# Performance work log

Hardware: AMD Instinct MI355X
Metric: run time of the kernel (lower is better)

## Reference

```python
import jax, jax.numpy as jnp
import numpy as np

L, D, H, KVH, DH, F, V, SMAX, T = 4, 2048, 16, 8, 128, 6144, 32000, 2048, 1024
EPS = 1e-6
ROPE_THETA = 1e6


def rotate_half(x, axis=-1):
    x1, x2 = jnp.split(x, 2, axis=axis)
    return jnp.concatenate((-x2, x1), axis=axis)


def rms(x, w):
    return w * (x / jnp.sqrt(jnp.mean(x * x, axis=-1, keepdims=True) + EPS))


def setup_inputs() -> dict:
    key = jax.random.key(0)
    ks = jax.random.split(key, 16)
    s = 0.02
    inv_freq = 1.0 / (ROPE_THETA ** (jnp.arange(0, DH, 2, dtype=jnp.float32) / DH))
    ang = jnp.arange(SMAX, dtype=jnp.float32)[:, None] * inv_freq[None, :]  # [SMAX, DH/2]
    cos_emb = jnp.concatenate([jnp.cos(ang), jnp.cos(ang)], axis=-1)  # [SMAX, DH]
    sin_emb = jnp.concatenate([jnp.sin(ang), jnp.sin(ang)], axis=-1)
    sf = DH ** (-0.25)  # scale_factor pre-baked into q_norm/k_norm weights
    return {
        "key_buffer": jnp.zeros((L, KVH, 1, DH, SMAX), jnp.float32),
        "value_buffer": jnp.zeros((L, KVH, 1, SMAX, DH), jnp.float32),
        "input_ids": jax.random.randint(ks[0], (1, T), 0, V, dtype=jnp.int32),
        "attention_mask": jnp.ones((1, T, T), jnp.float32),
        "past_len": 0,
        "embed_data": jax.random.randint(ks[1], (V, D), 0, 256).astype(jnp.uint8),
        "embed_scale": jax.random.uniform(ks[2], (V, 1), jnp.float32, 0.001, 0.02),
        "embed_zero": jax.random.normal(ks[3], (V, 1), jnp.float32) * 0.1,
        "cos_emb": cos_emb,
        "sin_emb": sin_emb,
        "w_in_ln": jnp.ones((L, D), jnp.float32),
        "Wq": jax.random.normal(ks[4], (L, D, H * DH), jnp.float32) * s,
        "Wk": jax.random.normal(ks[5], (L, D, KVH * DH), jnp.float32) * s,
        "Wv": jax.random.normal(ks[6], (L, D, KVH * DH), jnp.float32) * s,
        "w_q_norm": jnp.full((L, DH), sf, jnp.float32),
        "w_k_norm": jnp.full((L, DH), sf, jnp.float32),
        "Wo": jax.random.normal(ks[7], (L, H * DH, D), jnp.float32) * s,
        "w_post_ln": jnp.ones((L, D), jnp.float32),
        "Wgate": jax.random.normal(ks[8], (L, D, F), jnp.float32) * s,
        "Wup": jax.random.normal(ks[9], (L, D, F), jnp.float32) * s,
        "Wdown": jax.random.normal(ks[10], (L, F, D), jnp.float32) * s,
        "w_final_norm": jnp.ones((D,), jnp.float32),
        "W_lm": jax.random.normal(ks[11], (D, V), jnp.float32) * s,
    }


def reference(key_buffer, value_buffer, input_ids, attention_mask, past_len,
              embed_data, embed_scale, embed_zero, cos_emb, sin_emb,
              w_in_ln, Wq, Wk, Wv, w_q_norm, w_k_norm, Wo, w_post_ln,
              Wgate, Wup, Wdown, w_final_norm, W_lm):
    new_len = input_ids.shape[1]
    end = past_len + new_len  # static (past_len is a Python int)
    cos_q = cos_emb[past_len:end]  # [T, DH]
    sin_q = sin_emb[past_len:end]
    # uint8 embedding dequant: e * scale + zero_point
    hidden = embed_data[input_ids].astype(jnp.float32) * embed_scale[input_ids] + embed_zero[input_ids]  # [1,T,D]
    # causal mask: (1 - tril) * -128, sliced to [1, new_len, end], times user mask
    rows = jnp.arange(new_len) + past_len
    cols = jnp.arange(end)
    mask = jnp.where(cols[None, :] <= rows[:, None], 0.0, -128.0)[None] * attention_mask  # [1,T,end]
    G = H // KVH
    for i in range(L):
        hn = rms(hidden, w_in_ln[i])[0]  # [T, D]
        q = (hn @ Wq[i]).reshape(new_len, H, DH)
        q = jnp.transpose(rms(q, w_q_norm[i]), (1, 0, 2))  # [H,T,DH] (sqrt(scale) baked in w_q_norm)
        k = (hn @ Wk[i]).reshape(new_len, KVH, DH)
        k = jnp.transpose(rms(k, w_k_norm[i]), (1, 2, 0))  # [KVH,DH,T]
        v = jnp.transpose((hn @ Wv[i]).reshape(new_len, KVH, DH), (1, 0, 2))  # [KVH,T,DH]
        # RoPE on keys (rotate along DH axis=1)
        k = k * cos_q.T + rotate_half(k, axis=1) * sin_q.T
        key_buffer = jax.lax.dynamic_update_slice(key_buffer, k[None, :, None], (i, 0, 0, 0, past_len))
        value_buffer = jax.lax.dynamic_update_slice(value_buffer, v[None, :, None], (i, 0, 0, past_len, 0))
        # GQA expand: each kv head repeated G times consecutively
        k_exp = jnp.repeat(key_buffer[i, :, 0, :, :end], G, axis=0)  # [H,DH,end]
        v_exp = jnp.repeat(value_buffer[i, :, 0, :end, :], G, axis=0)  # [H,end,DH]
        q_rot = q * cos_q[None] + rotate_half(q, axis=-1) * sin_q[None]
        scores = jnp.einsum('htd,hds->hts', q_rot, k_exp) + mask
        attn = jax.nn.softmax(scores, axis=-1)
        ctx = jnp.transpose(jnp.einsum('hts,hsd->htd', attn, v_exp), (1, 0, 2)).reshape(1, new_len, H * DH)
        hidden = hidden + ctx @ Wo[i]
        hn2 = rms(hidden, w_post_ln[i])
        hidden = hidden + (jax.nn.silu(hn2 @ Wgate[i]) * (hn2 @ Wup[i])) @ Wdown[i]
    last = rms(hidden[:, -1], w_final_norm)  # [1, D]
    logits = last @ W_lm  # [1, V]
    tok_id = jnp.argmax(logits, axis=-1, keepdims=True).astype(jnp.int32)
    new_seq_len = jnp.array([end], dtype=jnp.int32)
    return (tok_id, key_buffer, value_buffer, new_seq_len)
```

## Files before the change

kernel.cpp:

```cpp
#include <hip/hip_runtime.h>
#include <cstdint>

#define L_ 4
#define D_ 2048
#define H_ 16
#define KVH_ 8
#define DH_ 128
#define F_ 6144
#define V_ 32000
#define SMAX_ 2048
#define T_ 1024
#define EPS_ 1e-6f
#define QB 64
#define SB 128

typedef unsigned short u16;
typedef unsigned int u32;
typedef float fvec4 __attribute__((ext_vector_type(4)));
typedef float f32x4 __attribute__((ext_vector_type(4)));
typedef __bf16 bf16x8 __attribute__((ext_vector_type(8)));

__device__ __forceinline__ u16 f2bf(float f) {
  union { float f; u32 u; } a; a.f = f;
  u32 u = a.u;
  return (u16)((u + 0x7FFFu + ((u >> 16) & 1u)) >> 16);
}

__device__ __forceinline__ void gld16(const void* g, void* l) {
  __builtin_amdgcn_global_load_lds(
      (const __attribute__((address_space(1))) void*)g,
      (__attribute__((address_space(3))) void*)l, 16, 0, 0);
}

__device__ __forceinline__ float blk_sum(float v, volatile float* sm) {
#pragma unroll
  for (int m = 32; m; m >>= 1) v += __shfl_xor(v, m);
  if ((threadIdx.x & 63) == 0) sm[threadIdx.x >> 6] = v;
  __syncthreads();
  v = sm[0] + sm[1] + sm[2] + sm[3];
  __syncthreads();
  return v;
}

__global__ void embed_k(const int* __restrict__ ids, const void* __restrict__ edata,
                        const float* __restrict__ esc, const float* __restrict__ ez,
                        float* __restrict__ hidden)
{
  const int* ei = (const int*)edata;
  int chk = ei[threadIdx.x & 63];
  bool ok = ((unsigned)chk) <= 255u;
  bool is_i32 = (__ballot(ok) == ~0ULL);
  int t = blockIdx.x;
  int id = ids[t];
  float sc = esc[id], zp = ez[id];
  size_t base = (size_t)id * D_;
  const uint8_t* eb = (const uint8_t*)edata;
  for (int d = threadIdx.x; d < D_; d += 256) {
    float e = is_i32 ? (float)ei[base + d] : (float)eb[base + d];
    hidden[(size_t)t * D_ + d] = e * sc + zp;
  }
}

__global__ __launch_bounds__(256)
void convT2_k(const float* __restrict__ W0, const float* __restrict__ W1,
              const float* __restrict__ W2,
              int x1, int x2, int N0, int N1, int N2,
              int r0, int r1, int r2, int K, u16* __restrict__ WT, int gu)
{
  __shared__ float tile[64][65];
  int x = blockIdx.x, k0 = blockIdx.y * 64;
  const float* W; int N, nb, rb;
  if (x < x1)      { W = W0; N = N0; nb = x;      rb = r0; }
  else if (x < x2) { W = W1; N = N1; nb = x - x1; rb = r1; }
  else             { W = W2; N = N2; nb = x - x2; rb = r2; }
  int n0 = nb * 64;
  int tid = threadIdx.x;
  int lk = tid >> 4, n4 = (tid & 15) * 4;
#pragma unroll
  for (int i = 0; i < 4; ++i) {
    int kr = i * 16 + lk;
    fvec4 v = *(const fvec4*)(W + (size_t)(k0 + kr) * N + n0 + n4);
#pragma unroll
    for (int j = 0; j < 4; ++j) tile[n4 + j][kr] = v[j];
  }
  __syncthreads();
  int n = tid >> 2, kq = (tid & 3) * 16;
  int f = n0 + n;
  int row = gu ? (rb + ((f >> 4) << 5) + (f & 15)) : (rb + f);
  union { u16 h[16]; uint4 q[2]; } o;
#pragma unroll
  for (int i = 0; i < 16; ++i) o.h[i] = f2bf(tile[n][kq + i]);
  u16* op = WT + (size_t)row * K + k0 + kq;
  *(uint4*)op = o.q[0];
  *(uint4*)(op + 8) = o.q[1];
}

template<int COMB>
__global__ void rms_k(float* __restrict__ x, const float* __restrict__ p0,
                      const float* __restrict__ p1, const float* __restrict__ w,
                      u16* __restrict__ out)
{
  __shared__ float sm[4];
  int t = blockIdx.x;
  fvec4* xr = (fvec4*)(x + (size_t)t * D_);
  fvec4 v0 = xr[threadIdx.x], v1 = xr[threadIdx.x + 256];
  if (COMB) {
    const fvec4* a = (const fvec4*)(p0 + (size_t)t * D_);
    const fvec4* b = (const fvec4*)(p1 + (size_t)t * D_);
    v0 += a[threadIdx.x] + b[threadIdx.x];
    v1 += a[threadIdx.x + 256] + b[threadIdx.x + 256];
    xr[threadIdx.x] = v0;
    xr[threadIdx.x + 256] = v1;
  }
  float s = v0[0]*v0[0] + v0[1]*v0[1] + v0[2]*v0[2] + v0[3]*v0[3]
          + v1[0]*v1[0] + v1[1]*v1[1] + v1[2]*v1[2] + v1[3]*v1[3];
  s = blk_sum(s, sm);
  float inv = rsqrtf(s * (1.f / D_) + EPS_);
  const fvec4* wr = (const fvec4*)w;
  fvec4 w0 = wr[threadIdx.x], w1 = wr[threadIdx.x + 256];
  u16* orow = out + (size_t)t * D_;
  uint2 o0, o1;
  o0.x = (u32)f2bf(w0[0]*v0[0]*inv) | ((u32)f2bf(w0[1]*v0[1]*inv) << 16);
  o0.y = (u32)f2bf(w0[2]*v0[2]*inv) | ((u32)f2bf(w0[3]*v0[3]*inv) << 16);
  o1.x = (u32)f2bf(w1[0]*v1[0]*inv) | ((u32)f2bf(w1[1]*v1[1]*inv) << 16);
  o1.y = (u32)f2bf(w1[2]*v1[2]*inv) | ((u32)f2bf(w1[3]*v1[3]*inv) << 16);
  *(uint2*)(orow + threadIdx.x * 4) = o0;
  *(uint2*)(orow + (threadIdx.x + 256) * 4) = o1;
}

template<int EPI>
__global__ __launch_bounds__(256)
void gemm_bt(const u16* __restrict__ A, const u16* __restrict__ B,
             float* __restrict__ Cf, u16* __restrict__ Cb,
             int K, int Ks, int ldC, long long zStride)
{
  __shared__ u16 lA[128 * 64];
  __shared__ u16 lB[128 * 64];
  const u16* Ab = A + (size_t)blockIdx.y * 128 * K;
  const u16* Bb = B + (size_t)blockIdx.x * 128 * K;
  int kz = blockIdx.z * Ks;

  int tid = threadIdx.x;
  int l = tid & 63;
  int wid = tid >> 6;
  int wr = wid >> 1, wc = wid & 1;
  int lrow = l & 15, lk = l >> 4;

  f32x4 acc[4][4] = {};

  for (int k0 = 0; k0 < Ks; k0 += 64) {
#pragma unroll
    for (int r = 0; r < 4; ++r) {
      int c = r * 256 + tid;
      int row = c >> 3, g = c & 7;
      int kel = kz + k0 + ((g ^ (row & 7)) << 3);
      gld16(Ab + (size_t)row * K + kel, (char*)lA + c * 16);
      gld16(Bb + (size_t)row * K + kel, (char*)lB + c * 16);
    }
    __syncthreads();
#pragma unroll
    for (int kk = 0; kk < 2; ++kk) {
      bf16x8 av[4], bv[4];
      int kbyte = (kk * 32 + lk * 8) * 2;
#pragma unroll
      for (int m = 0; m < 4; ++m) {
        int row = wr * 64 + m * 16 + lrow;
        int byt = (row * 128 + kbyte) ^ ((row & 7) << 4);
        av[m] = *(const bf16x8*)((const char*)lA + byt);
      }
#pragma unroll
      for (int n = 0; n < 4; ++n) {
        int row = wc * 64 + n * 16 + lrow;
        int byt = (row * 128 + kbyte) ^ ((row & 7) << 4);
        bv[n] = *(const bf16x8*)((const char*)lB + byt);
      }
#pragma unroll
      for (int m = 0; m < 4; ++m)
#pragma unroll
        for (int n = 0; n < 4; ++n)
          acc[m][n] = __builtin_amdgcn_mfma_f32_16x16x32_bf16(av[m], bv[n], acc[m][n], 0, 0, 0);
    }
    __syncthreads();
  }

  int grow0 = blockIdx.y * 128 + wr * 64 + lk * 4;
  if (EPI == 3) {
    int fcol0 = blockIdx.x * 64 + wc * 32 + lrow;
#pragma unroll
    for (int m = 0; m < 4; ++m)
#pragma unroll
      for (int np = 0; np < 2; ++np)
#pragma unroll
        for (int r = 0; r < 4; ++r) {
          float g = acc[m][2 * np][r], u = acc[m][2 * np + 1][r];
          float val = g / (1.f + __expf(-g)) * u;
          Cb[(size_t)(grow0 + m * 16 + r) * ldC + fcol0 + np * 16] = f2bf(val);
        }
    return;
  }
  float* Cz = Cf + (long long)blockIdx.z * zStride;
  int gcol0 = blockIdx.x * 128 + wc * 64 + lrow;
#pragma unroll
  for (int m = 0; m < 4; ++m)
#pragma unroll
    for (int n = 0; n < 4; ++n)
#pragma unroll
      for (int r = 0; r < 4; ++r) {
        size_t off = (size_t)(grow0 + m * 16 + r) * ldC + gcol0 + n * 16;
        Cz[off] = acc[m][n][r];
      }
}

__global__ __launch_bounds__(256)
void qkvpost_k(const float* __restrict__ p0, const float* __restrict__ p1,
               const float* __restrict__ wq, const float* __restrict__ wk,
               const float* __restrict__ cosT, const float* __restrict__ sinT,
               const int* __restrict__ plp,
               u16* __restrict__ qr, u16* __restrict__ kr, u16* __restrict__ vT,
               float* __restrict__ key_out, float* __restrict__ val_out)
{
  __shared__ float tile[64][132];
  int t0 = blockIdx.x * 64;
  int z = blockIdx.y;
  int pl = plp[0];
  int tid = threadIdx.x;
  int cb = z < 16 ? z * 128 : (z < 24 ? 2048 + (z - 16) * 128 : 3072 + (z - 24) * 128);

  {
    int r = tid >> 5;
    int c = (tid & 31) * 4;
#pragma unroll
    for (int i = 0; i < 8; ++i) {
      int row = i * 8 + r;
      size_t off = (size_t)(t0 + row) * 4096 + cb + c;
      fvec4 v = *(const fvec4*)(p0 + off) + *(const fvec4*)(p1 + off);
      *(fvec4*)&tile[row][c] = v;
    }
  }
  __syncthreads();

  if (z < 24) {
    int row = tid >> 2, q = tid & 3;
    int dbase = q * 32, pbase = (q ^ 2) * 32;
    const float* wn = z < 16 ? wq : wk;
    float sgn = (q < 2) ? -1.f : 1.f;
    fvec4 xv[8];
    float ss = 0.f;
#pragma unroll
    for (int j = 0; j < 8; ++j) {
      xv[j] = *(const fvec4*)&tile[row][dbase + j * 4];
      ss += xv[j][0]*xv[j][0] + xv[j][1]*xv[j][1] + xv[j][2]*xv[j][2] + xv[j][3]*xv[j][3];
    }
    ss += __shfl_xor(ss, 1);
    ss += __shfl_xor(ss, 2);
    float inv = rsqrtf(ss * (1.f / 128.f) + EPS_);
    int p = pl + t0 + row;
    float rv[32];
#pragma unroll
    for (int j = 0; j < 8; ++j) {
      fvec4 xo = *(const fvec4*)&tile[row][pbase + j * 4];
      fvec4 wv = *(const fvec4*)(wn + dbase + j * 4);
      fvec4 wo = *(const fvec4*)(wn + pbase + j * 4);
      fvec4 cs = *(const fvec4*)(cosT + (size_t)p * 128 + dbase + j * 4);
      fvec4 sn = *(const fvec4*)(sinT + (size_t)p * 128 + dbase + j * 4);
#pragma unroll
      for (int e = 0; e < 4; ++e) {
        float xn = wv[e] * xv[j][e] * inv;
        float xp = wo[e] * xo[e] * inv;
        rv[j * 4 + e] = xn * cs[e] + sgn * xp * sn[e];
      }
    }
    union { u32 w[8]; uint4 q4[2]; } ob;
    u16* orow = (z < 16 ? qr + ((size_t)z * T_ + t0 + row) * 128
                        : kr + ((size_t)(z - 16) * T_ + t0 + row) * 128) + dbase;
#pragma unroll
    for (int j = 0; j < 8; ++j)
      ob.w[j] = (u32)f2bf(rv[2 * j]) | ((u32)f2bf(rv[2 * j + 1]) << 16);
    *(uint4*)orow = ob.q4[0];
#pragma unroll
    for (int j = 0; j < 8; ++j)
      ob.w[j] = (u32)f2bf(rv[16 + 2 * j]) | ((u32)f2bf(rv[17 + 2 * j]) << 16);
    *(uint4*)(orow + 16) = ob.q4[0];

    if (z >= 16) {
      __syncthreads();
#pragma unroll
      for (int j = 0; j < 8; ++j) {
        fvec4 v; v[0] = rv[j*4]; v[1] = rv[j*4+1]; v[2] = rv[j*4+2]; v[3] = rv[j*4+3];
        *(fvec4*)&tile[row][dbase + j * 4] = v;
      }
      __syncthreads();
      int d = tid >> 1, cc = (tid & 1) * 32;
      float* kp = key_out + ((size_t)(z - 16) * 128 + d) * SMAX_ + pl + t0 + cc;
      if ((pl & 3) == 0) {
#pragma unroll
        for (int j4 = 0; j4 < 8; ++j4) {
          fvec4 v;
#pragma unroll
          for (int e = 0; e < 4; ++e) v[e] = tile[cc + j4 * 4 + e][d];
          *(fvec4*)(kp + j4 * 4) = v;
        }
      } else {
        for (int j = 0; j < 32; ++j) kp[j] = tile[cc + j][d];
      }
    }
  } else {
    int kv = z - 24;
    int row = tid >> 2, q = tid & 3;
    float* vp = val_out + ((size_t)kv * SMAX_ + pl + t0 + row) * 128 + q * 32;
#pragma unroll
    for (int j = 0; j < 8; ++j)
      *(fvec4*)(vp + j * 4) = *(const fvec4*)&tile[row][q * 32 + j * 4];
    int d = tid >> 1, cc = (tid & 1) * 32;
    union { u32 w[8]; uint4 q4[2]; } ob;
    u16* tp = vT + ((size_t)kv * 128 + d) * T_ + t0 + cc;
#pragma unroll
    for (int j = 0; j < 8; ++j)
      ob.w[j] = (u32)f2bf(tile[cc + 2 * j][d]) | ((u32)f2bf(tile[cc + 2 * j + 1][d]) << 16);
    *(uint4*)tp = ob.q4[0];
    *(uint4*)(tp + 8) = ob.q4[1];
  }
}

__global__ __launch_bounds__(256)
void flash_k(const u16* __restrict__ qr, const u16* __restrict__ kr,
             const u16* __restrict__ vTb, const float* __restrict__ am,
             const int* __restrict__ plp, u16* __restrict__ ctx)
{
  __shared__ u16 lQ[QB * DH_];
  __shared__ u16 lKV[SB * DH_];
  __shared__ u16 lP[QB * SB];
  __shared__ float lScale[QB];
  __shared__ float lSum[QB];

  int qt = gridDim.x - 1 - blockIdx.x;
  int h = blockIdx.y;
  int kvh = h >> 1;
  int pl = plp[0];
  int tid = threadIdx.x;
  int l = tid & 63, w = tid >> 6;
  int lrow = l & 15, lk = l >> 4;

  const u16* Qb = qr + ((size_t)h * T_ + qt * QB) * DH_;
  const u16* Kb = kr + (size_t)kvh * T_ * DH_;
  const u16* Vb = vTb + (size_t)kvh * DH_ * T_;

#pragma unroll
  for (int r = 0; r < 4; ++r) {
    int c = r * 256 + tid;
    int row = c >> 4, g = c & 15;
    gld16(Qb + (size_t)row * DH_ + ((g ^ (row & 7)) << 3), (char*)lQ + c * 16);
  }

  float m_run = -3.0e38f, l_run = 0.f;
  f32x4 acc_o[4][2] = {};

  int t_lo = qt * QB;
  int s_hi = min(T_, t_lo + QB + pl);
  int nt = (s_hi + SB - 1) / SB;
  int tcol = w * 16 + lrow;
  int tg = t_lo + tcol;

  for (int it = 0; it < nt; ++it) {
    int s0 = it * SB;
#pragma unroll
    for (int r = 0; r < 8; ++r) {
      int c = r * 256 + tid;
      int row = c >> 4, g = c & 15;
      gld16(Kb + (size_t)(s0 + row) * DH_ + ((g ^ (row & 7)) << 3), (char*)lKV + c * 16);
    }
    __syncthreads();

    f32x4 acc_s[8] = {};
#pragma unroll
    for (int kk = 0; kk < 4; ++kk) {
      int kbyte = kk * 64 + lk * 16;
      int trow = w * 16 + lrow;
      bf16x8 bq = *(const bf16x8*)((const char*)lQ + ((trow * 256 + kbyte) ^ ((trow & 7) << 4)));
#pragma unroll
      for (int m = 0; m < 8; ++m) {
        int srow = m * 16 + lrow;
        bf16x8 ak = *(const bf16x8*)((const char*)lKV + ((srow * 256 + kbyte) ^ ((srow & 7) << 4)));
        acc_s[m] = __builtin_amdgcn_mfma_f32_16x16x32_bf16(ak, bq, acc_s[m], 0, 0, 0);
      }
    }
    __syncthreads();

#pragma unroll
    for (int r = 0; r < 8; ++r) {
      int c = r * 256 + tid;
      int row = c >> 4, g = c & 15;
      gld16(Vb + (size_t)row * T_ + s0 + ((g ^ (row & 7)) << 3), (char*)lKV + c * 16);
    }

    bool full = (s0 + SB <= t_lo + pl + 1);
    float vmax = -3.0e38f;
    float sv[8][4];
    if (full) {
#pragma unroll
      for (int m = 0; m < 8; ++m)
#pragma unroll
        for (int r = 0; r < 4; ++r) {
          float val = acc_s[m][r]; sv[m][r] = val; vmax = fmaxf(vmax, val);
        }
    } else {
#pragma unroll
      for (int m = 0; m < 8; ++m) {
        int sg = s0 + m * 16 + lk * 4;
        fvec4 a4 = *(const fvec4*)(am + (size_t)tg * T_ + sg);
#pragma unroll
        for (int r = 0; r < 4; ++r) {
          float val = acc_s[m][r] + ((sg + r <= tg + pl) ? 0.f : -128.f * a4[r]);
          sv[m][r] = val; vmax = fmaxf(vmax, val);
        }
      }
    }
    vmax = fmaxf(vmax, __shfl_xor(vmax, 16));
    vmax = fmaxf(vmax, __shfl_xor(vmax, 32));
    float m_new = fmaxf(m_run, vmax);
    float corr = __expf(m_run - m_new);
    float psum = 0.f;
    u32 pw[8][2];
#pragma unroll
    for (int m = 0; m < 8; ++m) {
      float pq0 = __expf(sv[m][0] - m_new);
      float pq1 = __expf(sv[m][1] - m_new);
      float pq2 = __expf(sv[m][2] - m_new);
      float pq3 = __expf(sv[m][3] - m_new);
      psum += (pq0 + pq1) + (pq2 + pq3);
      pw[m][0] = (u32)f2bf(pq0) | ((u32)f2bf(pq1) << 16);
      pw[m][1] = (u32)f2bf(pq2) | ((u32)f2bf(pq3) << 16);
    }
    psum += __shfl_xor(psum, 16);
    psum += __shfl_xor(psum, 32);
    l_run = l_run * corr + psum;
    m_run = m_new;
    if (lk == 0) lScale[tcol] = corr;
#pragma unroll
    for (int m = 0; m < 8; ++m) {
      int byt = (tcol * 256 + m * 32 + lk * 8) ^ ((tcol & 7) << 4);
      *(uint2*)((char*)lP + byt) = make_uint2(pw[m][0], pw[m][1]);
    }
    __syncthreads();

#pragma unroll
    for (int m = 0; m < 4; ++m) {
      fvec4 c4 = *(const fvec4*)&lScale[m * 16 + lk * 4];
#pragma unroll
      for (int n = 0; n < 2; ++n)
#pragma unroll
        for (int r = 0; r < 4; ++r) acc_o[m][n][r] *= c4[r];
    }
#pragma unroll
    for (int kk = 0; kk < 4; ++kk) {
      int kbyte = kk * 64 + lk * 16;
      bf16x8 ap[4], bv[2];
#pragma unroll
      for (int m = 0; m < 4; ++m) {
        int trow = m * 16 + lrow;
        ap[m] = *(const bf16x8*)((const char*)lP + ((trow * 256 + kbyte) ^ ((trow & 7) << 4)));
      }
#pragma unroll
      for (int n = 0; n < 2; ++n) {
        int drow = w * 32 + n * 16 + lrow;
        bv[n] = *(const bf16x8*)((const char*)lKV + ((drow * 256 + kbyte) ^ ((drow & 7) << 4)));
      }
#pragma unroll
      for (int m = 0; m < 4; ++m)
#pragma unroll
        for (int n = 0; n < 2; ++n)
          acc_o[m][n] = __builtin_amdgcn_mfma_f32_16x16x32_bf16(ap[m], bv[n], acc_o[m][n], 0, 0, 0);
    }
    __syncthreads();
  }

  if (lk == 0) lSum[tcol] = l_run;
  __syncthreads();
#pragma unroll
  for (int m = 0; m < 4; ++m) {
    fvec4 s4 = *(const fvec4*)&lSum[m * 16 + lk * 4];
#pragma unroll
    for (int r = 0; r < 4; ++r) {
      float inv = 1.f / s4[r];
      int trow = t_lo + m * 16 + lk * 4 + r;
      u16* crow = ctx + (size_t)trow * (H_ * DH_) + h * DH_;
#pragma unroll
      for (int n = 0; n < 2; ++n) {
        int d = w * 32 + n * 16 + lrow;
        crow[d] = f2bf(acc_o[m][n][r] * inv);
      }
    }
  }
}

__global__ void frms_k(const float* __restrict__ x, const float* __restrict__ p0,
                       const float* __restrict__ p1, const float* __restrict__ w,
                       float* __restrict__ out)
{
  __shared__ float sm[4];
  float s = 0.f;
  for (int d = threadIdx.x; d < D_; d += 256) {
    float v = x[d] + p0[d] + p1[d];
    s += v * v;
  }
  s = blk_sum(s, sm);
  float inv = rsqrtf(s * (1.f / D_) + EPS_);
  for (int d = threadIdx.x; d < D_; d += 256)
    out[d] = w[d] * (x[d] + p0[d] + p1[d]) * inv;
}

__global__ void lmgemv_k(const float* __restrict__ last, const float* __restrict__ Wlm,
                         float* __restrict__ part)
{
  __shared__ float ls[256];
  int v = blockIdx.x * 256 + threadIdx.x;
  int c = blockIdx.y;
  ls[threadIdx.x] = last[c * 256 + threadIdx.x];
  __syncthreads();
  const float* Wp = Wlm + (size_t)c * 256 * V_ + v;
  float acc = 0.f;
#pragma unroll 8
  for (int d = 0; d < 256; d++) acc += ls[d] * Wp[(size_t)d * V_];
  part[(size_t)c * V_ + v] = acc;
}

__global__ void amax_part_k(const float* __restrict__ part, float2* __restrict__ out)
{
  __shared__ float sv[4];
  __shared__ int si[4];
  int v = blockIdx.x * 256 + threadIdx.x;
  float val = 0.f;
#pragma unroll
  for (int c = 0; c < 8; c++) val += part[(size_t)c * V_ + v];
  float bv = val; int bi = v;
#pragma unroll
  for (int m = 32; m; m >>= 1) {
    float ov = __shfl_xor(bv, m);
    int oi = __shfl_xor(bi, m);
    if (ov > bv || (ov == bv && oi < bi)) { bv = ov; bi = oi; }
  }
  if ((threadIdx.x & 63) == 0) { sv[threadIdx.x >> 6] = bv; si[threadIdx.x >> 6] = bi; }
  __syncthreads();
  if (threadIdx.x == 0) {
    for (int w = 1; w < 4; w++)
      if (sv[w] > bv || (sv[w] == bv && si[w] < bi)) { bv = sv[w]; bi = si[w]; }
    out[blockIdx.x] = make_float2(bv, (float)bi);
  }
}

__global__ void finalize_k(const float2* __restrict__ part, int np,
                           const int* __restrict__ plp, float* __restrict__ dout,
                           unsigned long long lastoff)
{
  if (threadIdx.x == 0) {
    float bv = part[0].x; int bi = (int)part[0].y;
    for (int b = 1; b < np; b++) {
      float v = part[b].x; int i = (int)part[b].y;
      if (v > bv || (v == bv && i < bi)) { bv = v; bi = i; }
    }
    dout[0] = (float)bi;
    dout[lastoff] = (float)(plp[0] + T_);
  }
}

extern "C" void kernel_launch(void* const* d_in, const int* in_sizes, int n_in,
                              void* d_out, int out_size, void* d_ws, size_t ws_size,
                              hipStream_t stream)
{
  (void)in_sizes; (void)n_in; (void)out_size; (void)ws_size;

  const float* key_in  = (const float*)d_in[0];
  const float* val_in  = (const float*)d_in[1];
  const int*   ids     = (const int*)d_in[2];
  const float* am      = (const float*)d_in[3];
  const int*   plp     = (const int*)d_in[4];
  const void*  edata   = d_in[5];
  const float* esc     = (const float*)d_in[6];
  const float* ez      = (const float*)d_in[7];
  const float* cosT    = (const float*)d_in[8];
  const float* sinT    = (const float*)d_in[9];
  const float* w_in_ln = (const float*)d_in[10];
  const float* Wq      = (const float*)d_in[11];
  const float* Wk      = (const float*)d_in[12];
  const float* Wv      = (const float*)d_in[13];
  const float* wqn     = (const float*)d_in[14];
  const float* wkn     = (const float*)d_in[15];
  const float* Wo      = (const float*)d_in[16];
  const float* wpost   = (const float*)d_in[17];
  const float* Wg      = (const float*)d_in[18];
  const float* Wu      = (const float*)d_in[19];
  const float* Wd      = (const float*)d_in[20];
  const float* wfin    = (const float*)d_in[21];
  const float* Wlm     = (const float*)d_in[22];

  float* out = (float*)d_out;
  const size_t KVN = (size_t)L_ * KVH_ * DH_ * SMAX_;
  float* key_out = out + 1;
  float* val_out = out + 1 + KVN;
  unsigned long long lastoff = 1 + 2 * KVN;

  char* ws = (char*)d_ws;
  u16*   wT     = (u16*)  (ws + 0);
  u16*   hn     = (u16*)  (ws + 50331648);
  float* P0     = (float*)(ws + 54525952);
  float* P1     = (float*)(ws + 71303168);
  u16*   qr     = (u16*)  (ws + 88080384);
  u16*   kr     = (u16*)  (ws + 92274688);
  u16*   vT     = (u16*)  (ws + 94371840);
  u16*   ctx    = (u16*)  (ws + 96468992);
  float* hidden = (float*)(ws + 100663296);
  u16*   mlp    = (u16*)  (ws + 109051904);
  float* last   = (float*)(ws + 121634816);
  float* lpart  = (float*)(ws + 121643008);
  float2* amaxp = (float2*)(ws + 122667008);

  const long long ZS = 4194304;

  hipMemcpyAsync(key_out, key_in, KVN * sizeof(float), hipMemcpyDeviceToDevice, stream);
  hipMemcpyAsync(val_out, val_in, KVN * sizeof(float), hipMemcpyDeviceToDevice, stream);
  embed_k<<<T_, 256, 0, stream>>>(ids, edata, esc, ez, hidden);

  for (int i = 0; i < L_; i++) {
    if (i == 0)
      rms_k<0><<<T_, 256, 0, stream>>>(hidden, nullptr, nullptr, w_in_ln, hn);
    else
      rms_k<1><<<T_, 256, 0, stream>>>(hidden, P0, P1, w_in_ln + (size_t)i * D_, hn);

    convT2_k<<<dim3(64, 32), 256, 0, stream>>>(
        Wq + (size_t)i * 4194304, Wk + (size_t)i * 2097152, Wv + (size_t)i * 2097152,
        32, 48, 2048, 1024, 1024, 0, 2048, 3072, 2048, wT, 0);
    gemm_bt<0><<<dim3(32, 8, 2), 256, 0, stream>>>(hn, wT, P0, nullptr, 2048, 1024, 4096, ZS);

    qkvpost_k<<<dim3(T_ / 64, 32), 256, 0, stream>>>(P0, P1,
        wqn + (size_t)i * DH_, wkn + (size_t)i * DH_, cosT, sinT, plp,
        qr, kr, vT,
        key_out + (size_t)i * KVH_ * DH_ * SMAX_,
        val_out + (size_t)i * KVH_ * SMAX_ * DH_);

    flash_k<<<dim3(T_ / QB, H_), 256, 0, stream>>>(qr, kr, vT, am, plp, ctx);

    convT2_k<<<dim3(32, 32), 256, 0, stream>>>(
        Wo + (size_t)i * 4194304, nullptr, nullptr,
        32, 64, 2048, 2048, 2048, 0, 0, 0, 2048, wT, 0);
    gemm_bt<0><<<dim3(16, 8, 2), 256, 0, stream>>>(ctx, wT, P0, nullptr, 2048, 1024, 2048, ZS);

    rms_k<1><<<T_, 256, 0, stream>>>(hidden, P0, P1, wpost + (size_t)i * D_, hn);

    convT2_k<<<dim3(192, 32), 256, 0, stream>>>(
        Wg + (size_t)i * 12582912, Wu + (size_t)i * 12582912, Wu + (size_t)i * 12582912,
        96, 192, 6144, 6144, 6144, 0, 16, 16, 2048, wT, 1);
    gemm_bt<3><<<dim3(96, 8, 1), 256, 0, stream>>>(hn, wT, nullptr, mlp, 2048, 2048, 6144, 0);

    convT2_k<<<dim3(32, 96), 256, 0, stream>>>(
        Wd + (size_t)i * 12582912, nullptr, nullptr,
        32, 64, 2048, 2048, 2048, 0, 0, 0, 6144, wT, 0);
    gemm_bt<0><<<dim3(16, 8, 2), 256, 0, stream>>>(mlp, wT, P0, nullptr, 6144, 3072, 2048, ZS);
  }

  frms_k<<<1, 256, 0, stream>>>(hidden + (size_t)(T_ - 1) * D_,
                                P0 + (size_t)(T_ - 1) * D_, P1 + (size_t)(T_ - 1) * D_,
                                wfin, last);
  lmgemv_k<<<dim3(V_ / 256, 8), 256, 0, stream>>>(last, Wlm, lpart);
  amax_part_k<<<V_ / 256, 256, 0, stream>>>(lpart, amaxp);
  finalize_k<<<1, 64, 0, stream>>>(amaxp, V_ / 256, plp, out, lastoff);
}
```

Baseline: 1.291 ms.

## Halve flash query tile, split S across waves, widen split-K to four partials

The flash attention kernel drops to 32-row query tiles, with the four waves split into two query groups by two key halves. Row max and sum are combined through shared memory, which doubles the number of blocks for better CU occupancy. The Wo and Wdown GEMMs now use four split-K partials instead of two, and the RMS kernels sum all four partials, raising parallelism at the cost of more partial-buffer traffic. The qkvpost kernel also adds the second 16-byte store for each output chunk, fixing previously unwritten elements.

```diff
diff --git a/kernel.cpp b/kernel.cpp
--- a/kernel.cpp
+++ b/kernel.cpp
@@ -11,8 +11,9 @@
 #define SMAX_ 2048
 #define T_ 1024
 #define EPS_ 1e-6f
-#define QB 64
+#define QB 32
 #define SB 128
+#define ZSE 4194304
 
 typedef unsigned short u16;
 typedef unsigned int u32;
@@ -95,20 +96,21 @@
   *(uint4*)(op + 8) = o.q[1];
 }
 
-template<int COMB>
-__global__ void rms_k(float* __restrict__ x, const float* __restrict__ p0,
-                      const float* __restrict__ p1, const float* __restrict__ w,
-                      u16* __restrict__ out)
+template<int NZ>
+__global__ void rms_k(float* __restrict__ x, const float* __restrict__ p,
+                      const float* __restrict__ w, u16* __restrict__ out)
 {
   __shared__ float sm[4];
   int t = blockIdx.x;
   fvec4* xr = (fvec4*)(x + (size_t)t * D_);
   fvec4 v0 = xr[threadIdx.x], v1 = xr[threadIdx.x + 256];
-  if (COMB) {
-    const fvec4* a = (const fvec4*)(p0 + (size_t)t * D_);
-    const fvec4* b = (const fvec4*)(p1 + (size_t)t * D_);
-    v0 += a[threadIdx.x] + b[threadIdx.x];
-    v1 += a[threadIdx.x + 256] + b[threadIdx.x + 256];
+  if (NZ > 0) {
+#pragma unroll
+    for (int z = 0; z < NZ; ++z) {
+      const fvec4* a = (const fvec4*)(p + (size_t)z * ZSE + (size_t)t * D_);
+      v0 += a[threadIdx.x];
+      v1 += a[threadIdx.x + 256];
+    }
     xr[threadIdx.x] = v0;
     xr[threadIdx.x + 256] = v1;
   }
@@ -277,10 +279,12 @@
     for (int j = 0; j < 8; ++j)
       ob.w[j] = (u32)f2bf(rv[2 * j]) | ((u32)f2bf(rv[2 * j + 1]) << 16);
     *(uint4*)orow = ob.q4[0];
+    *(uint4*)(orow + 8) = ob.q4[1];
 #pragma unroll
     for (int j = 0; j < 8; ++j)
       ob.w[j] = (u32)f2bf(rv[16 + 2 * j]) | ((u32)f2bf(rv[17 + 2 * j]) << 16);
     *(uint4*)(orow + 16) = ob.q4[0];
+    *(uint4*)(orow + 24) = ob.q4[1];
 
     if (z >= 16) {
       __syncthreads();
@@ -330,8 +334,10 @@
   __shared__ u16 lQ[QB * DH_];
   __shared__ u16 lKV[SB * DH_];
   __shared__ u16 lP[QB * SB];
+  __shared__ float lMax[2][2][16];
+  __shared__ float lSum[2][2][16];
   __shared__ float lScale[QB];
-  __shared__ float lSum[QB];
+  __shared__ float lFin[QB];
 
   int qt = gridDim.x - 1 - blockIdx.x;
   int h = blockIdx.y;
@@ -340,25 +346,26 @@
   int tid = threadIdx.x;
   int l = tid & 63, w = tid >> 6;
   int lrow = l & 15, lk = l >> 4;
+  int tb = w & 1, sh = w >> 1;
+  int tcol = tb * 16 + lrow;
 
   const u16* Qb = qr + ((size_t)h * T_ + qt * QB) * DH_;
   const u16* Kb = kr + (size_t)kvh * T_ * DH_;
   const u16* Vb = vTb + (size_t)kvh * DH_ * T_;
 
 #pragma unroll
-  for (int r = 0; r < 4; ++r) {
+  for (int r = 0; r < 2; ++r) {
     int c = r * 256 + tid;
     int row = c >> 4, g = c & 15;
     gld16(Qb + (size_t)row * DH_ + ((g ^ (row & 7)) << 3), (char*)lQ + c * 16);
   }
 
   float m_run = -3.0e38f, l_run = 0.f;
-  f32x4 acc_o[4][2] = {};
+  f32x4 acc_o[2][2] = {};
 
   int t_lo = qt * QB;
   int s_hi = min(T_, t_lo + QB + pl);
   int nt = (s_hi + SB - 1) / SB;
-  int tcol = w * 16 + lrow;
   int tg = t_lo + tcol;
 
   for (int it = 0; it < nt; ++it) {
@@ -371,15 +378,15 @@
     }
     __syncthreads();
 
-    f32x4 acc_s[8] = {};
+    f32x4 acc_s[4] = {};
 #pragma unroll
     for (int kk = 0; kk < 4; ++kk) {
       int kbyte = kk * 64 + lk * 16;
-      int trow = w * 16 + lrow;
+      int trow = tb * 16 + lrow;
       bf16x8 bq = *(const bf16x8*)((const char*)lQ + ((trow * 256 + kbyte) ^ ((trow & 7) << 4)));
 #pragma unroll
-      for (int m = 0; m < 8; ++m) {
-        int srow = m * 16 + lrow;
+      for (int m = 0; m < 4; ++m) {
+        int srow = sh * 64 + m * 16 + lrow;
         bf16x8 ak = *(const bf16x8*)((const char*)lKV + ((srow * 256 + kbyte) ^ ((srow & 7) << 4)));
         acc_s[m] = __builtin_amdgcn_mfma_f32_16x16x32_bf16(ak, bq, acc_s[m], 0, 0, 0);
       }
@@ -394,19 +401,19 @@
     }
 
     bool full = (s0 + SB <= t_lo + pl + 1);
+    float sv[4][4];
     float vmax = -3.0e38f;
-    float sv[8][4];
     if (full) {
 #pragma unroll
-      for (int m = 0; m < 8; ++m)
+      for (int m = 0; m < 4; ++m)
 #pragma unroll
         for (int r = 0; r < 4; ++r) {
           float val = acc_s[m][r]; sv[m][r] = val; vmax = fmaxf(vmax, val);
         }
     } else {
 #pragma unroll
-      for (int m = 0; m < 8; ++m) {
-        int sg = s0 + m * 16 + lk * 4;
+      for (int m = 0; m < 4; ++m) {
+        int sg = s0 + sh * 64 + m * 16 + lk * 4;
         fvec4 a4 = *(const fvec4*)(am + (size_t)tg * T_ + sg);
 #pragma unroll
         for (int r = 0; r < 4; ++r) {
@@ -417,34 +424,39 @@
     }
     vmax = fmaxf(vmax, __shfl_xor(vmax, 16));
     vmax = fmaxf(vmax, __shfl_xor(vmax, 32));
-    float m_new = fmaxf(m_run, vmax);
+    if (lk == 0) lMax[tb][sh][lrow] = vmax;
+    __syncthreads();
+
+    float om = fmaxf(lMax[tb][0][lrow], lMax[tb][1][lrow]);
+    float m_new = fmaxf(m_run, om);
     float corr = __expf(m_run - m_new);
     float psum = 0.f;
-    u32 pw[8][2];
-#pragma unroll
-    for (int m = 0; m < 8; ++m) {
-      float pq0 = __expf(sv[m][0] - m_new);
-      float pq1 = __expf(sv[m][1] - m_new);
-      float pq2 = __expf(sv[m][2] - m_new);
-      float pq3 = __expf(sv[m][3] - m_new);
-      psum += (pq0 + pq1) + (pq2 + pq3);
-      pw[m][0] = (u32)f2bf(pq0) | ((u32)f2bf(pq1) << 16);
-      pw[m][1] = (u32)f2bf(pq2) | ((u32)f2bf(pq3) << 16);
+    u32 pw[4][2];
+#pragma unroll
+    for (int m = 0; m < 4; ++m) {
+      float p0 = __expf(sv[m][0] - m_new);
+      float p1 = __expf(sv[m][1] - m_new);
+      float p2 = __expf(sv[m][2] - m_new);
+      float p3 = __expf(sv[m][3] - m_new);
+      psum += (p0 + p1) + (p2 + p3);
+      pw[m][0] = (u32)f2bf(p0) | ((u32)f2bf(p1) << 16);
+      pw[m][1] = (u32)f2bf(p2) | ((u32)f2bf(p3) << 16);
     }
     psum += __shfl_xor(psum, 16);
     psum += __shfl_xor(psum, 32);
-    l_run = l_run * corr + psum;
+    if (lk == 0) lSum[tb][sh][lrow] = psum;
+    if (lk == 0 && sh == 0) lScale[tcol] = corr;
+#pragma unroll
+    for (int m = 0; m < 4; ++m) {
+      int byt = (tcol * 256 + sh * 128 + m * 32 + lk * 8) ^ ((tcol & 7) << 4);
+      *(uint2*)((char*)lP + byt) = make_uint2(pw[m][0], pw[m][1]);
+    }
+    __syncthreads();
+
+    l_run = l_run * corr + lSum[tb][0][lrow] + lSum[tb][1][lrow];
     m_run = m_new;
-    if (lk == 0) lScale[tcol] = corr;
-#pragma unroll
-    for (int m = 0; m < 8; ++m) {
-      int byt = (tcol * 256 + m * 32 + lk * 8) ^ ((tcol & 7) << 4);
-      *(uint2*)((char*)lP + byt) = make_uint2(pw[m][0], pw[m][1]);
-    }
-    __syncthreads();
-
-#pragma unroll
-    for (int m = 0; m < 4; ++m) {
+#pragma unroll
+    for (int m = 0; m < 2; ++m) {
       fvec4 c4 = *(const fvec4*)&lScale[m * 16 + lk * 4];
 #pragma unroll
       for (int n = 0; n < 2; ++n)
@@ -454,9 +466,9 @@
 #pragma unroll
     for (int kk = 0; kk < 4; ++kk) {
       int kbyte = kk * 64 + lk * 16;
-      bf16x8 ap[4], bv[2];
-#pragma unroll
-      for (int m = 0; m < 4; ++m) {
+      bf16x8 ap[2], bv[2];
+#pragma unroll
+      for (int m = 0; m < 2; ++m) {
         int trow = m * 16 + lrow;
         ap[m] = *(const bf16x8*)((const char*)lP + ((trow * 256 + kbyte) ^ ((trow & 7) << 4)));
       }
@@ -466,7 +478,7 @@
         bv[n] = *(const bf16x8*)((const char*)lKV + ((drow * 256 + kbyte) ^ ((drow & 7) << 4)));
       }
 #pragma unroll
-      for (int m = 0; m < 4; ++m)
+      for (int m = 0; m < 2; ++m)
 #pragma unroll
         for (int n = 0; n < 2; ++n)
           acc_o[m][n] = __builtin_amdgcn_mfma_f32_16x16x32_bf16(ap[m], bv[n], acc_o[m][n], 0, 0, 0);
@@ -474,11 +486,11 @@
     __syncthreads();
   }
 
-  if (lk == 0) lSum[tcol] = l_run;
+  if (lk == 0 && sh == 0) lFin[tcol] = l_run;
   __syncthreads();
 #pragma unroll
-  for (int m = 0; m < 4; ++m) {
-    fvec4 s4 = *(const fvec4*)&lSum[m * 16 + lk * 4];
+  for (int m = 0; m < 2; ++m) {
+    fvec4 s4 = *(const fvec4*)&lFin[m * 16 + lk * 4];
 #pragma unroll
     for (int r = 0; r < 4; ++r) {
       float inv = 1.f / s4[r];
@@ -493,20 +505,19 @@
   }
 }
 
-__global__ void frms_k(const float* __restrict__ x, const float* __restrict__ p0,
-                       const float* __restrict__ p1, const float* __restrict__ w,
-                       float* __restrict__ out)
+__global__ void frms_k(const float* __restrict__ x, const float* __restrict__ p,
+                       const float* __restrict__ w, float* __restrict__ out)
 {
   __shared__ float sm[4];
   float s = 0.f;
   for (int d = threadIdx.x; d < D_; d += 256) {
-    float v = x[d] + p0[d] + p1[d];
+    float v = x[d] + p[d] + p[ZSE + d] + p[2 * ZSE + d] + p[3 * ZSE + d];
     s += v * v;
   }
   s = blk_sum(s, sm);
   float inv = rsqrtf(s * (1.f / D_) + EPS_);
   for (int d = threadIdx.x; d < D_; d += 256)
-    out[d] = w[d] * (x[d] + p0[d] + p1[d]) * inv;
+    out[d] = w[d] * (x[d] + p[d] + p[ZSE + d] + p[2 * ZSE + d] + p[3 * ZSE + d]) * inv;
 }
 
 __global__ void lmgemv_k(const float* __restrict__ last, const float* __restrict__ Wlm,
@@ -602,19 +613,16 @@
   char* ws = (char*)d_ws;
   u16*   wT     = (u16*)  (ws + 0);
   u16*   hn     = (u16*)  (ws + 50331648);
-  float* P0     = (float*)(ws + 54525952);
-  float* P1     = (float*)(ws + 71303168);
-  u16*   qr     = (u16*)  (ws + 88080384);
-  u16*   kr     = (u16*)  (ws + 92274688);
-  u16*   vT     = (u16*)  (ws + 94371840);
-  u16*   ctx    = (u16*)  (ws + 96468992);
-  float* hidden = (float*)(ws + 100663296);
-  u16*   mlp    = (u16*)  (ws + 109051904);
-  float* last   = (float*)(ws + 121634816);
-  float* lpart  = (float*)(ws + 121643008);
-  float2* amaxp = (float2*)(ws + 122667008);
-
-  const long long ZS = 4194304;
+  float* P      = (float*)(ws + 54525952);
+  u16*   qr     = (u16*)  (ws + 121634816);
+  u16*   kr     = (u16*)  (ws + 125829120);
+  u16*   vT     = (u16*)  (ws + 127926272);
+  u16*   ctx    = (u16*)  (ws + 130023424);
+  float* hidden = (float*)(ws + 134217728);
+  u16*   mlp    = (u16*)  (ws + 142606336);
+  float* last   = (float*)(ws + 155189248);
+  float* lpart  = (float*)(ws + 155197440);
+  float2* amaxp = (float2*)(ws + 156221440);
 
   hipMemcpyAsync(key_out, key_in, KVN * sizeof(float), hipMemcpyDeviceToDevice, stream);
   hipMemcpyAsync(val_out, val_in, KVN * sizeof(float), hipMemcpyDeviceToDevice, stream);
@@ -622,16 +630,16 @@
 
   for (int i = 0; i < L_; i++) {
     if (i == 0)
-      rms_k<0><<<T_, 256, 0, stream>>>(hidden, nullptr, nullptr, w_in_ln, hn);
+      rms_k<0><<<T_, 256, 0, stream>>>(hidden, nullptr, w_in_ln, hn);
     else
-      rms_k<1><<<T_, 256, 0, stream>>>(hidden, P0, P1, w_in_ln + (size_t)i * D_, hn);
+      rms_k<4><<<T_, 256, 0, stream>>>(hidden, P, w_in_ln + (size_t)i * D_, hn);
 
     convT2_k<<<dim3(64, 32), 256, 0, stream>>>(
         Wq + (size_t)i * 4194304, Wk + (size_t)i * 2097152, Wv + (size_t)i * 2097152,
         32, 48, 2048, 1024, 1024, 0, 2048, 3072, 2048, wT, 0);
-    gemm_bt<0><<<dim3(32, 8, 2), 256, 0, stream>>>(hn, wT, P0, nullptr, 2048, 1024, 4096, ZS);
-
-    qkvpost_k<<<dim3(T_ / 64, 32), 256, 0, stream>>>(P0, P1,
+    gemm_bt<0><<<dim3(32, 8, 2), 256, 0, stream>>>(hn, wT, P, nullptr, 2048, 1024, 4096, ZSE);
+
+    qkvpost_k<<<dim3(T_ / 64, 32), 256, 0, stream>>>(P, P + ZSE,
         wqn + (size_t)i * DH_, wkn + (size_t)i * DH_, cosT, sinT, plp,
         qr, kr, vT,
         key_out + (size_t)i * KVH_ * DH_ * SMAX_,
@@ -642,9 +650,9 @@
     convT2_k<<<dim3(32, 32), 256, 0, stream>>>(
         Wo + (size_t)i * 4194304, nullptr, nullptr,
         32, 64, 2048, 2048, 2048, 0, 0, 0, 2048, wT, 0);
-    gemm_bt<0><<<dim3(16, 8, 2), 256, 0, stream>>>(ctx, wT, P0, nullptr, 2048, 1024, 2048, ZS);
-
-    rms_k<1><<<T_, 256, 0, stream>>>(hidden, P0, P1, wpost + (size_t)i * D_, hn);
+    gemm_bt<0><<<dim3(16, 8, 4), 256, 0, stream>>>(ctx, wT, P, nullptr, 2048, 512, 2048, ZSE);
+
+    rms_k<4><<<T_, 256, 0, stream>>>(hidden, P, wpost + (size_t)i * D_, hn);
 
     convT2_k<<<dim3(192, 32), 256, 0, stream>>>(
         Wg + (size_t)i * 12582912, Wu + (size_t)i * 12582912, Wu + (size_t)i * 12582912,
@@ -654,12 +662,11 @@
     convT2_k<<<dim3(32, 96), 256, 0, stream>>>(
         Wd + (size_t)i * 12582912, nullptr, nullptr,
         32, 64, 2048, 2048, 2048, 0, 0, 0, 6144, wT, 0);
-    gemm_bt<0><<<dim3(16, 8, 2), 256, 0, stream>>>(mlp, wT, P0, nullptr, 6144, 3072, 2048, ZS);
+    gemm_bt<0><<<dim3(16, 8, 4), 256, 0, stream>>>(mlp, wT, P, nullptr, 6144, 1536, 2048, ZSE);
   }
 
   frms_k<<<1, 256, 0, stream>>>(hidden + (size_t)(T_ - 1) * D_,
-                                P0 + (size_t)(T_ - 1) * D_, P1 + (size_t)(T_ - 1) * D_,
-                                wfin, last);
+                                P + (size_t)(T_ - 1) * D_, wfin, last);
   lmgemv_k<<<dim3(V_ / 256, 8), 256, 0, stream>>>(last, Wlm, lpart);
   amax_part_k<<<V_ / 256, 256, 0, stream>>>(lpart, amaxp);
   finalize_k<<<1, 64, 0, stream>>>(amaxp, V_ / 256, plp, out, lastoff);
```

Result: faster. 1.199 ms (-7.2%).
